# Optimization experiments

Measured on AMD Instinct MI355X. Metric: run time of the kernel, lower is better.

Reference implementation:

```python
import jax, jax.numpy as jnp
import numpy as np

POOLED_SIZES = [12, 16, 20, 24]
NUM_HEADS = 8
EPS_LN = 1e-5


def _pool_mat(in_size, out_size):
    # torch adaptive_avg_pool1d/2d semantics as an averaging matrix [out, in]
    m = np.zeros((out_size, in_size), np.float32)
    for i in range(out_size):
        s = (i * in_size) // out_size
        e = -((-(i + 1) * in_size) // out_size)  # ceil
        m[i, s:e] = 1.0 / (e - s)
    return jnp.asarray(m)


def _dwconv(x, w, b):
    # depthwise 3x3, stride 1, padding 1 (NCHW, OIHW with I=1)
    y = jax.lax.conv_general_dilated(
        x, w, (1, 1), 'SAME', feature_group_count=x.shape[1],
        dimension_numbers=('NCHW', 'OIHW', 'NCHW'))
    return y + b[None, :, None, None]


def _ln(x, g, b):
    m = x.mean(-1, keepdims=True)
    v = jnp.mean((x - m) ** 2, axis=-1, keepdims=True)
    return (x - m) / jnp.sqrt(v + EPS_LN) * g + b


def setup_inputs() -> dict:
    key = jax.random.key(0)
    ks = jax.random.split(key, 16)
    B, H, W, C = 4, 56, 56, 256
    hid = 4 * C
    nrm = lambda k, shape, s=0.02: jax.random.normal(k, shape, jnp.float32) * s
    inp = {
        'x': jax.random.normal(ks[0], (B, H * W, C), jnp.float32),
        'cpe_w': nrm(ks[1], (C, 1, 3, 3)), 'cpe_b': jnp.zeros((C,), jnp.float32),
        'norm1_w': jnp.ones((C,), jnp.float32), 'norm1_b': jnp.zeros((C,), jnp.float32),
        'q_w': nrm(ks[2], (C, C)),
        'kv_w': nrm(ks[3], (2 * C, C)),
        'attn_norm_w': jnp.ones((C,), jnp.float32), 'attn_norm_b': jnp.zeros((C,), jnp.float32),
        'proj_w': nrm(ks[4], (C, C)), 'proj_b': jnp.zeros((C,), jnp.float32),
        'norm2_w': jnp.ones((C,), jnp.float32), 'norm2_b': jnp.zeros((C,), jnp.float32),
        'fc1_w': nrm(ks[5], (hid, C)), 'fc1_b': jnp.zeros((hid,), jnp.float32),
        'irb_conv_w': nrm(ks[6], (hid, 1, 3, 3)), 'irb_conv_b': jnp.zeros((hid,), jnp.float32),
        'fc2_w': nrm(ks[7], (C, hid)), 'fc2_b': jnp.zeros((C,), jnp.float32),
        'H': H, 'W': W,
    }
    for i in range(4):
        inp[f'dconv{i}_w'] = nrm(ks[8 + i], (C, 1, 3, 3))
        inp[f'dconv{i}_b'] = jnp.zeros((C,), jnp.float32)
    return inp


def _forward(x, cpe_w, cpe_b, norm1_w, norm1_b, q_w, kv_w, attn_norm_w, attn_norm_b,
             proj_w, proj_b, dconv0_w, dconv0_b, dconv1_w, dconv1_b, dconv2_w, dconv2_b,
             dconv3_w, dconv3_b, norm2_w, norm2_b, fc1_w, fc1_b, irb_conv_w, irb_conv_b,
             fc2_w, fc2_b, H, W):
    B, N, C = x.shape
    nh = NUM_HEADS
    hd = C // nh
    scale = hd ** -0.5
    # conditional positional encoding: x = cpe(x) + x
    xi = x.transpose(0, 2, 1).reshape(B, C, H, W)
    xi = _dwconv(xi, cpe_w, cpe_b) + xi
    x = xi.reshape(B, C, N).transpose(0, 2, 1)
    # ---- pyramid pooling attention ----
    xn = _ln(x, norm1_w, norm1_b)
    q = (xn @ q_w.T).reshape(B, N, nh, hd).transpose(0, 2, 1, 3)  # [B,nh,N,hd]
    x_ = xn.transpose(0, 2, 1).reshape(B, C, H, W)
    dws = [(dconv0_w, dconv0_b), (dconv1_w, dconv1_b),
           (dconv2_w, dconv2_b), (dconv3_w, dconv3_b)]
    pools = []
    for p, (dw, db) in zip(POOLED_SIZES, dws):
        ph = _pool_mat(H, p)
        pw = _pool_mat(W, p)
        pool = jnp.einsum('oi,bcij,pj->bcop', ph, x_, pw)  # adaptive avg pool (p,p)
        pool = pool + _dwconv(pool, dw, db)
        pools.append(pool.reshape(B, C, -1))
    pools = jnp.concatenate(pools, axis=2).transpose(0, 2, 1)  # [B,P,C], P=1376
    pools = _ln(pools, attn_norm_w, attn_norm_b)
    kv = (pools @ kv_w.T).reshape(B, -1, 2, nh, hd).transpose(2, 0, 3, 1, 4)
    k, v = kv[0], kv[1]  # [B,nh,P,hd]
    attn = jax.nn.softmax(jnp.einsum('bhnd,bhpd->bhnp', q, k) * scale, axis=-1)
    out = jnp.einsum('bhnp,bhpd->bhnd', attn, v).transpose(0, 2, 1, 3).reshape(B, N, C)
    out = out @ proj_w.T + proj_b
    x = x + out
    # ---- IRB FFN ----
    xn = _ln(x, norm2_w, norm2_b)
    xi = xn.transpose(0, 2, 1).reshape(B, C, H, W)
    h = jnp.einsum('oc,bchw->bohw', fc1_w, xi) + fc1_b[None, :, None, None]
    h = jax.nn.gelu(h, approximate=False)
    h = h + _dwconv(h, irb_conv_w, irb_conv_b)
    o = jnp.einsum('oc,bchw->bohw', fc2_w, h) + fc2_b[None, :, None, None]
    x = x + o.reshape(B, C, N).transpose(0, 2, 1)
    return x


def reference(x, cpe_w, cpe_b, norm1_w, norm1_b, q_w, kv_w, attn_norm_w, attn_norm_b,
              proj_w, proj_b, dconv0_w, dconv0_b, dconv1_w, dconv1_b, dconv2_w, dconv2_b,
              dconv3_w, dconv3_b, norm2_w, norm2_b, fc1_w, fc1_b, irb_conv_w, irb_conv_b,
              fc2_w, fc2_b, H, W):
    return _forward(x, cpe_w, cpe_b, norm1_w, norm1_b, q_w, kv_w, attn_norm_w, attn_norm_b,
                    proj_w, proj_b, dconv0_w, dconv0_b, dconv1_w, dconv1_b, dconv2_w, dconv2_b,
                    dconv3_w, dconv3_b, norm2_w, norm2_b, fc1_w, fc1_b, irb_conv_w, irb_conv_b,
                    fc2_w, fc2_b, H, W)
```

## Files before the change

kernel.cpp:

```cpp
#include <hip/hip_runtime.h>
#include <hip/hip_bf16.h>

#define BQ 4
#define HH 56
#define WW 56
#define NN (HH*WW)
#define CC 256
#define NHEAD 8
#define HD 32
#define PP 1376
#define PPAD 1408
#define HIDN 1024
#define EPS_LN 1e-5f
#define QSCALE_LOG2E 0.25503484f

typedef unsigned short bf16u;
typedef __attribute__((ext_vector_type(8))) short short8;
typedef __attribute__((ext_vector_type(4))) float f32x4;

__device__ __forceinline__ float bf2f(bf16u u){
  union { unsigned int i; float f; } v; v.i = ((unsigned int)u) << 16; return v.f;
}
__device__ __forceinline__ bf16u f2bf(float f){
  unsigned int x = __float_as_uint(f);
  x += 0x7fffu + ((x >> 16) & 1u);
  return (bf16u)(x >> 16);
}
__device__ __forceinline__ bf16u f2bf_r(float f){
  return (bf16u)((__float_as_uint(f) + 0x8000u) >> 16);
}
__device__ __forceinline__ void cvt4(const ushort4 u, float* d){
  d[0]=bf2f(u.x); d[1]=bf2f(u.y); d[2]=bf2f(u.z); d[3]=bf2f(u.w);
}

#define CSEG 4
__global__ void k_init(const float* __restrict__ qw, const float* __restrict__ kvw,
                       const float* __restrict__ pw, const float* __restrict__ f1,
                       const float* __restrict__ f2, bf16u* __restrict__ wo,
                       const float* __restrict__ x, const float* __restrict__ w,
                       const float* __restrict__ bias, const float* __restrict__ g,
                       const float* __restrict__ be, float* __restrict__ x1,
                       bf16u* __restrict__ xnb){
  if (blockIdx.x < 768){
    int off = (blockIdx.x*256 + threadIdx.x) * 4;
    const float* s;
    if (off < 65536)       s = qw  + off;
    else if (off < 196608) s = kvw + off - 65536;
    else if (off < 262144) s = pw  + off - 196608;
    else if (off < 524288) s = f1  + off - 262144;
    else                   s = f2  + off - 524288;
    float4 v = *(const float4*)s;
    ushort4 u = {f2bf(v.x), f2bf(v.y), f2bf(v.z), f2bf(v.w)};
    *(ushort4*)(wo + off) = u;
    return;
  }
  int t = threadIdx.x;
  int wave = t >> 6, lane = t & 63;
  int widx = (blockIdx.x - 768)*4 + wave;
  const int nseg = WW/CSEG;
  int xseg = widx % nseg;
  int y    = (widx / nseg) % HH;
  int b    = widx / (nseg*HH);
  int c0 = lane*4;
  int x0 = xseg*CSEG;
  float wv[36];
  {
    const float* wp = w + (size_t)c0*9;
#pragma unroll
    for (int i = 0; i < 9; i++){
      float4 v = *(const float4*)(wp + i*4);
      wv[i*4+0]=v.x; wv[i*4+1]=v.y; wv[i*4+2]=v.z; wv[i*4+3]=v.w;
    }
  }
  float4 bi4 = *(const float4*)&bias[c0];
  float bi[4] = {bi4.x, bi4.y, bi4.z, bi4.w};
  float4 gv = *(const float4*)&g[c0];
  float4 bv = *(const float4*)&be[c0];
  const float* rowc = x + ((size_t)b*NN + (size_t)y*WW)*CC + c0;
  const float* rowm = (y > 0)    ? rowc - (size_t)WW*CC : rowc;
  const float* rowp = (y < HH-1) ? rowc + (size_t)WW*CC : rowc;
  if (y == 0){
#pragma unroll
    for (int cc = 0; cc < 4; cc++){ wv[cc*9+0]=0.f; wv[cc*9+1]=0.f; wv[cc*9+2]=0.f; }
  }
  if (y == HH-1){
#pragma unroll
    for (int cc = 0; cc < 4; cc++){ wv[cc*9+6]=0.f; wv[cc*9+7]=0.f; wv[cc*9+8]=0.f; }
  }
  float win[3][3][4];
  float4 rawA[3], rawB[3];
  if (x0 == 0){
#pragma unroll
    for (int r = 0; r < 3; r++)
#pragma unroll
      for (int cc = 0; cc < 4; cc++) win[0][r][cc] = 0.f;
  } else {
    size_t o = (size_t)(x0-1)*CC;
    float4 a0 = *(const float4*)&rowm[o];
    float4 a1 = *(const float4*)&rowc[o];
    float4 a2 = *(const float4*)&rowp[o];
    win[0][0][0]=a0.x; win[0][0][1]=a0.y; win[0][0][2]=a0.z; win[0][0][3]=a0.w;
    win[0][1][0]=a1.x; win[0][1][1]=a1.y; win[0][1][2]=a1.z; win[0][1][3]=a1.w;
    win[0][2][0]=a2.x; win[0][2][1]=a2.y; win[0][2][2]=a2.z; win[0][2][3]=a2.w;
  }
  {
    size_t o = (size_t)x0*CC;
    float4 a0 = *(const float4*)&rowm[o];
    float4 a1 = *(const float4*)&rowc[o];
    float4 a2 = *(const float4*)&rowp[o];
    win[1][0][0]=a0.x; win[1][0][1]=a0.y; win[1][0][2]=a0.z; win[1][0][3]=a0.w;
    win[1][1][0]=a1.x; win[1][1][1]=a1.y; win[1][1][2]=a1.z; win[1][1][3]=a1.w;
    win[1][2][0]=a2.x; win[1][2][1]=a2.y; win[1][2][2]=a2.z; win[1][2][3]=a2.w;
  }
  {
    size_t o = (size_t)(x0+1)*CC;
    rawA[0] = *(const float4*)&rowm[o];
    rawA[1] = *(const float4*)&rowc[o];
    rawA[2] = *(const float4*)&rowp[o];
  }
#pragma unroll
  for (int xx = 0; xx < CSEG; xx++){
    float4* cur = (xx & 1) ? rawB : rawA;
    float4* nxt = (xx & 1) ? rawA : rawB;
    if (xx < CSEG-1){
      int xg = x0 + xx + 2;
      if (xg < WW){
        size_t o = (size_t)xg*CC;
        nxt[0] = *(const float4*)&rowm[o];
        nxt[1] = *(const float4*)&rowc[o];
        nxt[2] = *(const float4*)&rowp[o];
      } else {
        float4 z = {0.f,0.f,0.f,0.f};
        nxt[0] = z; nxt[1] = z; nxt[2] = z;
      }
    }
    int sl2 = (xx+2)%3, slm = xx%3, slc = (xx+1)%3;
#pragma unroll
    for (int r = 0; r < 3; r++){
      win[sl2][r][0]=cur[r].x; win[sl2][r][1]=cur[r].y;
      win[sl2][r][2]=cur[r].z; win[sl2][r][3]=cur[r].w;
    }
    float o4[4];
#pragma unroll
    for (int cc = 0; cc < 4; cc++){
      float a = bi[cc];
      a += win[slm][0][cc]*wv[cc*9+0] + win[slc][0][cc]*wv[cc*9+1] + win[sl2][0][cc]*wv[cc*9+2];
      a += win[slm][1][cc]*wv[cc*9+3] + win[slc][1][cc]*wv[cc*9+4] + win[sl2][1][cc]*wv[cc*9+5];
      a += win[slm][2][cc]*wv[cc*9+6] + win[slc][2][cc]*wv[cc*9+7] + win[sl2][2][cc]*wv[cc*9+8];
      o4[cc] = win[slc][1][cc] + a;
    }
    size_t pix = (size_t)b*NN + (size_t)y*WW + x0 + xx;
    float4 ov = {o4[0],o4[1],o4[2],o4[3]};
    *(float4*)&x1[pix*CC + c0] = ov;
    float s  = o4[0]+o4[1]+o4[2]+o4[3];
    float s2 = o4[0]*o4[0]+o4[1]*o4[1]+o4[2]*o4[2]+o4[3]*o4[3];
#pragma unroll
    for (int off = 32; off; off >>= 1){
      s  += __shfl_xor(s,  off);
      s2 += __shfl_xor(s2, off);
    }
    float mean = s * (1.f/CC);
    float var  = s2 * (1.f/CC) - mean*mean;
    float rstd = rsqrtf(var + EPS_LN);
    float y0 = (o4[0]-mean)*rstd*gv.x + bv.x;
    float y1 = (o4[1]-mean)*rstd*gv.y + bv.y;
    float y2 = (o4[2]-mean)*rstd*gv.z + bv.z;
    float y3 = (o4[3]-mean)*rstd*gv.w + bv.w;
    ushort4 yb = {f2bf_r(y0), f2bf_r(y1), f2bf_r(y2), f2bf_r(y3)};
    *(ushort4*)&xnb[pix*CC + c0] = yb;
  }
}

__global__ void k_ln_bf16(const float* __restrict__ X, const float* __restrict__ g,
                          const float* __restrict__ be, bf16u* __restrict__ Y){
  int wave = threadIdx.x >> 6, lane = threadIdx.x & 63;
  int row = blockIdx.x*4 + wave;
  int c0 = lane*4;
  float4 v = *(const float4*)&X[(size_t)row*CC + c0];
  float s  = v.x+v.y+v.z+v.w;
  float s2 = v.x*v.x+v.y*v.y+v.z*v.z+v.w*v.w;
#pragma unroll
  for (int off = 32; off; off >>= 1){
    s  += __shfl_xor(s,  off);
    s2 += __shfl_xor(s2, off);
  }
  float mean = s * (1.f/CC);
  float var  = s2 * (1.f/CC) - mean*mean;
  float rstd = rsqrtf(var + EPS_LN);
  float4 gv = *(const float4*)&g[c0];
  float4 bv = *(const float4*)&be[c0];
  ushort4 yb = {f2bf_r((v.x-mean)*rstd*gv.x + bv.x),
                f2bf_r((v.y-mean)*rstd*gv.y + bv.y),
                f2bf_r((v.z-mean)*rstd*gv.z + bv.z),
                f2bf_r((v.w-mean)*rstd*gv.w + bv.w)};
  *(ushort4*)&Y[(size_t)row*CC + c0] = yb;
}

__global__ void k_pool(const bf16u* __restrict__ xnb, float* __restrict__ praw){
  int bp = blockIdx.x;
  int b = bp / PP, p = bp % PP;
  int ps, pi;
  if (p < 144)      { ps = 12; pi = p; }
  else if (p < 400) { ps = 16; pi = p - 144; }
  else if (p < 800) { ps = 20; pi = p - 400; }
  else              { ps = 24; pi = p - 800; }
  int oi = pi / ps, oj = pi % ps;
  int si = oi*HH/ps, ei = ((oi+1)*HH + ps - 1)/ps;
  int sj = oj*WW/ps, ej = ((oj+1)*WW + ps - 1)/ps;
  int c = threadIdx.x;
  const bf16u* xb = xnb + (size_t)b*NN*CC + c;
  float acc = 0.f;
  for (int i = si; i < ei; i++)
    for (int j = sj; j < ej; j++)
      acc += bf2f(xb[(size_t)(i*WW+j)*CC]);
  praw[(size_t)bp*CC + c] = acc / (float)((ei-si)*(ej-sj));
}

__global__ void k_pooldw_ln(const float* __restrict__ praw,
    const float* w0, const float* b0, const float* w1, const float* b1,
    const float* w2, const float* b2, const float* w3, const float* b3,
    const float* __restrict__ g, const float* __restrict__ be,
    bf16u* __restrict__ pools){
  int bp = blockIdx.x;
  int b = bp / PP, p = bp % PP;
  int ps, pi, off; const float *w, *bi;
  if (p < 144)      { ps=12; pi=p;     off=0;   w=w0; bi=b0; }
  else if (p < 400) { ps=16; pi=p-144; off=144; w=w1; bi=b1; }
  else if (p < 800) { ps=20; pi=p-400; off=400; w=w2; bi=b2; }
  else              { ps=24; pi=p-800; off=800; w=w3; bi=b3; }
  int oi = pi/ps, oj = pi%ps;
  int c = threadIdx.x;
  const float* base = praw + (size_t)(b*PP + off)*CC + c;
  float acc = bi[c];
#pragma unroll
  for (int kh = 0; kh < 3; kh++){
    int ii = oi + kh - 1; if (ii < 0 || ii >= ps) continue;
#pragma unroll
    for (int kw = 0; kw < 3; kw++){
      int jj = oj + kw - 1; if (jj < 0 || jj >= ps) continue;
      acc += base[(size_t)(ii*ps+jj)*CC] * w[c*9 + kh*3 + kw];
    }
  }
  float v = base[(size_t)(oi*ps+oj)*CC] + acc;
  float s = v, s2 = v*v;
#pragma unroll
  for (int o2_ = 32; o2_; o2_ >>= 1){
    s  += __shfl_down(s,  o2_);
    s2 += __shfl_down(s2, o2_);
  }
  __shared__ float red[10];
  int wv_ = c >> 6, ln = c & 63;
  if (ln == 0){ red[wv_] = s; red[4+wv_] = s2; }
  __syncthreads();
  if (c == 0){
    float S  = red[0]+red[1]+red[2]+red[3];
    float S2 = red[4]+red[5]+red[6]+red[7];
    float mean = S * (1.f/CC);
    float var  = S2 * (1.f/CC) - mean*mean;
    red[8] = mean; red[9] = rsqrtf(var + EPS_LN);
  }
  __syncthreads();
  float mean = red[8], rstd = red[9];
  pools[(size_t)bp*CC + c] = f2bf_r((v - mean) * rstd * g[c] + be[c]);
}

#define GST 40
template<int MT, int NT, bool OUT_BF16, bool HAS_BIAS, bool DO_GELU, bool HAS_RES, bool VT_OUT>
__global__ __launch_bounds__(256) void k_gemm_mfma(const bf16u* __restrict__ A,
                       const bf16u* __restrict__ Wt,
                       const float* __restrict__ bias, void* Outp,
                       const float* Res, bf16u* __restrict__ vtout,
                       int M, int Nout, int K, float oscale){
  constexpr int MW = (MT == 128) ? 4 : 2;
  constexpr int NW = (NT == 128) ? 4 : 2;
  __shared__ bf16u Ash[2][MT*GST];
  __shared__ bf16u Bsh[2][NT*GST];
  int t = threadIdx.x;
  int wave = t >> 6, lane = t & 63, quad = lane >> 4, l16 = lane & 15;
  int m0 = blockIdx.y * MT, n0 = blockIdx.x * NT;
  int wm = (wave >> 1) * (MT/2);
  int wn = (wave & 1) * (NT/2);
  int ar = (MT==128) ? (t>>1) : (t>>2);
  int ac = (MT==128) ? ((t&1)*16) : ((t&3)*8);
  int br = (NT==128) ? (t>>1) : (t>>2);
  int bc = (NT==128) ? ((t&1)*16) : ((t&3)*8);
  int astore = ar*GST + ac;
  int bstore = br*GST + bc;
  const bf16u* ap = A  + (size_t)(m0+ar)*K + ac;
  const bf16u* bp = Wt + (size_t)(n0+br)*K + bc;

  {
    uint4 t0 = *(const uint4*)ap;
    *(uint4*)&Ash[0][astore] = t0;
    if constexpr (MT == 128){ uint4 t1 = *(const uint4*)(ap+8); *(uint4*)&Ash[0][astore+8] = t1; }
    uint4 t2 = *(const uint4*)bp;
    *(uint4*)&Bsh[0][bstore] = t2;
    if constexpr (NT == 128){ uint4 t3 = *(const uint4*)(bp+8); *(uint4*)&Bsh[0][bstore+8] = t3; }
  }
  uint4 aA0, aA1, bA0, bA1;
  uint4 aB0, aB1, bB0, bB1;
  ap += 32; bp += 32;
  aA0 = *(const uint4*)ap;
  if constexpr (MT == 128) aA1 = *(const uint4*)(ap+8);
  bA0 = *(const uint4*)bp;
  if constexpr (NT == 128) bA1 = *(const uint4*)(bp+8);
  ap += 32; bp += 32;
  aB0 = *(const uint4*)ap;
  if constexpr (MT == 128) aB1 = *(const uint4*)(ap+8);
  bB0 = *(const uint4*)bp;
  if constexpr (NT == 128) bB1 = *(const uint4*)(bp+8);
  ap += 32; bp += 32;
  __syncthreads();

  f32x4 zero = {0.f,0.f,0.f,0.f};
  f32x4 acc[MW][NW];
#pragma unroll
  for (int i = 0; i < MW; i++)
#pragma unroll
    for (int j = 0; j < NW; j++) acc[i][j] = zero;

  int nks = K >> 5;

#define GEMM_STEP(BUF) { \
    short8 af[MW], bfr[NW]; \
    _Pragma("unroll") \
    for (int mi = 0; mi < MW; mi++) \
      af[mi] = *(const short8*)&Ash[BUF][(wm + mi*16 + l16)*GST + quad*8]; \
    _Pragma("unroll") \
    for (int ni = 0; ni < NW; ni++) \
      bfr[ni] = *(const short8*)&Bsh[BUF][(wn + ni*16 + l16)*GST + quad*8]; \
    _Pragma("unroll") \
    for (int mi = 0; mi < MW; mi++) \
      _Pragma("unroll") \
      for (int ni = 0; ni < NW; ni++) \
        acc[mi][ni] = __builtin_amdgcn_mfma_f32_16x16x32_bf16(af[mi], bfr[ni], acc[mi][ni], 0,0,0); }

  for (int ks = 0; ks < nks; ks += 2){
    if (ks < nks-1){
      *(uint4*)&Ash[1][astore] = aA0;
      if constexpr (MT == 128) *(uint4*)&Ash[1][astore+8] = aA1;
      *(uint4*)&Bsh[1][bstore] = bA0;
      if constexpr (NT == 128) *(uint4*)&Bsh[1][bstore+8] = bA1;
      if (ks < nks-3){
        aA0 = *(const uint4*)ap;
        if constexpr (MT == 128) aA1 = *(const uint4*)(ap+8);
        bA0 = *(const uint4*)bp;
        if constexpr (NT == 128) bA1 = *(const uint4*)(bp+8);
        ap += 32; bp += 32;
      }
    }
    GEMM_STEP(0)
    if (ks < nks-1) __syncthreads();
    if (ks+1 < nks-1){
      *(uint4*)&Ash[0][astore] = aB0;
      if constexpr (MT == 128) *(uint4*)&Ash[0][astore+8] = aB1;
      *(uint4*)&Bsh[0][bstore] = bB0;
      if constexpr (NT == 128) *(uint4*)&Bsh[0][bstore+8] = bB1;
      if (ks+1 < nks-3){
        aB0 = *(const uint4*)ap;
        if constexpr (MT == 128) aB1 = *(const uint4*)(ap+8);
        bB0 = *(const uint4*)bp;
        if constexpr (NT == 128) bB1 = *(const uint4*)(bp+8);
        ap += 32; bp += 32;
      }
    }
    if (ks+1 < nks){
      GEMM_STEP(1)
      if (ks+1 < nks-1) __syncthreads();
    }
  }
#undef GEMM_STEP

#pragma unroll
  for (int mi = 0; mi < MW; mi++){
#pragma unroll
    for (int r = 0; r < 4; r++){
      int row = m0 + wm + mi*16 + quad*4 + r;
#pragma unroll
      for (int ni = 0; ni < NW; ni++){
        int col = n0 + wn + ni*16 + l16;
        float v = acc[mi][ni][r] * oscale;
        if constexpr (HAS_BIAS) v += bias[col];
        if constexpr (DO_GELU)  v = 0.5f*v*(1.f + erff(v*0.70710678118654752f));
        if constexpr (HAS_RES)  v += Res[(size_t)row*Nout + col];
        if constexpr (VT_OUT){
          if (col < CC){
            ((bf16u*)Outp)[(size_t)row*Nout + col] = f2bf_r(v);
          } else {
            int bb = row / PP, pp = row - bb*PP;
            vtout[((size_t)(bb*CC + (col - CC)))*PPAD + pp] = f2bf_r(v);
          }
        } else if constexpr (OUT_BF16){
          ((bf16u*)Outp)[(size_t)row*Nout + col] = f2bf_r(v);
        } else {
          ((float*)Outp)[(size_t)row*Nout + col] = v;
        }
      }
    }
  }
}

#define KST 40
#define VST 72
__global__ __launch_bounds__(256) void k_attn_mfma(const bf16u* __restrict__ q,
                       const bf16u* __restrict__ kvb, const bf16u* __restrict__ vt,
                       bf16u* __restrict__ out){
  __shared__ bf16u Ksh[2][64*KST];
  __shared__ bf16u Vsh[2][32*VST];
  int t = threadIdx.x;
  int wave = t >> 6, lane = t & 63, quad = lane >> 4, l16 = lane & 15;
  int bid = blockIdx.x;
  int qt = bid % (NN/64);
  int h  = (bid / (NN/64)) % NHEAD;
  int b  = bid / ((NN/64)*NHEAD);
  int q0 = qt*64 + wave*16;
  const bf16u* qptr = q + (size_t)(b*NN + q0 + l16)*CC + h*HD + quad*8;
  short8 qf = *(const short8*)qptr;
  f32x4 zero = {0.f,0.f,0.f,0.f};
  f32x4 o0 = zero, o1 = zero, osum = zero;
  const short8 onesf = {0x3F80,0x3F80,0x3F80,0x3F80,0x3F80,0x3F80,0x3F80,0x3F80};
  int ksr = t >> 2, ksc = (t & 3) * 8;
  int vsr = t >> 3, vsc = (t & 7) * 8;
  const bf16u* ksrc = kvb + (size_t)(b*PP + ksr)*(2*CC) + h*HD + ksc;
  const bf16u* vsrc = vt  + (size_t)(b*CC + h*HD + vsr)*PPAD + vsc;
  int krow = (ksr & 32) | ((ksr & 4) << 2) | ((ksr & 24) >> 1) | (ksr & 3);
  int kstore = krow*KST + ksc;
  int vstore = vsr*VST + vsc;
  int koffA = l16*KST + quad*8;
  int koffB = koffA + 16*KST;
  int voff0 = l16*VST + quad*8;
  int voff1 = (16 + l16)*VST + quad*8;

  uint4 kreg = *(const uint4*)ksrc;
  uint4 vreg = *(const uint4*)vsrc;
  *(uint4*)&Ksh[0][kstore] = kreg;
  *(uint4*)&Vsh[0][vstore] = vreg;
  ksrc += (size_t)64*(2*CC); vsrc += 64;
  kreg = *(const uint4*)ksrc; vreg = *(const uint4*)vsrc;
  __syncthreads();

#define PAIR(KB, VB, cb) { \
    short8 kfa = *(const short8*)&KB[cb*KST + koffA]; \
    short8 kfb = *(const short8*)&KB[cb*KST + koffB]; \
    f32x4 sa = __builtin_amdgcn_mfma_f32_16x16x32_bf16(kfa, qf, zero, 0,0,0); \
    f32x4 sb = __builtin_amdgcn_mfma_f32_16x16x32_bf16(kfb, qf, zero, 0,0,0); \
    float ea0 = __builtin_amdgcn_exp2f(sa[0]), ea1 = __builtin_amdgcn_exp2f(sa[1]); \
    float ea2 = __builtin_amdgcn_exp2f(sa[2]), ea3 = __builtin_amdgcn_exp2f(sa[3]); \
    float eb0 = __builtin_amdgcn_exp2f(sb[0]), eb1 = __builtin_amdgcn_exp2f(sb[1]); \
    float eb2 = __builtin_amdgcn_exp2f(sb[2]), eb3 = __builtin_amdgcn_exp2f(sb[3]); \
    unsigned ra0 = __float_as_uint(ea0) + 0x8000u, ra1 = __float_as_uint(ea1) + 0x8000u; \
    unsigned ra2 = __float_as_uint(ea2) + 0x8000u, ra3 = __float_as_uint(ea3) + 0x8000u; \
    unsigned rb0 = __float_as_uint(eb0) + 0x8000u, rb1 = __float_as_uint(eb1) + 0x8000u; \
    unsigned rb2 = __float_as_uint(eb2) + 0x8000u, rb3 = __float_as_uint(eb3) + 0x8000u; \
    union { uint4 u; short8 s; } pk; \
    pk.u.x = __builtin_amdgcn_perm(ra1, ra0, 0x07060302u); \
    pk.u.y = __builtin_amdgcn_perm(ra3, ra2, 0x07060302u); \
    pk.u.z = __builtin_amdgcn_perm(rb1, rb0, 0x07060302u); \
    pk.u.w = __builtin_amdgcn_perm(rb3, rb2, 0x07060302u); \
    short8 pa = pk.s; \
    short8 vf0 = *(const short8*)&VB[cb + voff0]; \
    short8 vf1 = *(const short8*)&VB[cb + voff1]; \
    o0 = __builtin_amdgcn_mfma_f32_16x16x32_bf16(pa, vf0, o0, 0,0,0); \
    o1 = __builtin_amdgcn_mfma_f32_16x16x32_bf16(pa, vf1, o1, 0,0,0); \
    osum = __builtin_amdgcn_mfma_f32_16x16x32_bf16(pa, onesf, osum, 0,0,0); }

  for (int ch = 0; ch < PPAD/64 - 1; ch++){
    int cur = ch & 1;
    bf16u* KB = &Ksh[cur][0];
    bf16u* VB = &Vsh[cur][0];
    *(uint4*)&Ksh[cur^1][kstore] = kreg;
    *(uint4*)&Vsh[cur^1][vstore] = vreg;
    if (ch < PPAD/64 - 2){
      ksrc += (size_t)64*(2*CC); vsrc += 64;
      kreg = *(const uint4*)ksrc; vreg = *(const uint4*)vsrc;
    }
    PAIR(KB, VB, 0)
    PAIR(KB, VB, 32)
    __syncthreads();
  }
  {
    bf16u* KB = &Ksh[1][0];
    bf16u* VB = &Vsh[1][0];
    PAIR(KB, VB, 0)
  }
#undef PAIR

#pragma unroll
  for (int r = 0; r < 4; r++){
    int qq = quad*4 + r;
    float inv = 1.f / osum[r];
    size_t base = (size_t)(b*NN + q0 + qq)*CC + h*HD;
    out[base + l16]      = f2bf_r(o0[r]*inv);
    out[base + 16 + l16] = f2bf_r(o1[r]*inv);
  }
}

#define DWSEG 8
__global__ __launch_bounds__(256) void k_dwh(const bf16u* __restrict__ h, const float* __restrict__ w,
                      const float* __restrict__ bias, bf16u* __restrict__ h2){
  const int nseg = WW/DWSEG;
  int bid = blockIdx.x;
  int xseg = bid % nseg;
  int y    = (bid / nseg) % HH;
  int b    = bid / (nseg*HH);
  int t = threadIdx.x;
  int c0 = t*4;
  int x0 = xseg*DWSEG;
  float wv[36];
  {
    const float4* wp = (const float4*)(w + (size_t)c0*9);
#pragma unroll
    for (int i = 0; i < 9; i++){
      float4 v = wp[i];
      wv[i*4+0]=v.x; wv[i*4+1]=v.y; wv[i*4+2]=v.z; wv[i*4+3]=v.w;
    }
  }
  float4 bi4 = *(const float4*)&bias[c0];
  float bi[4] = {bi4.x, bi4.y, bi4.z, bi4.w};
  const bf16u* rowc = h + ((size_t)b*NN + (size_t)y*WW)*HIDN + c0;
  const bf16u* rowm = (y > 0)    ? rowc - (size_t)WW*HIDN : rowc;
  const bf16u* rowp = (y < HH-1) ? rowc + (size_t)WW*HIDN : rowc;
  if (y == 0){
#pragma unroll
    for (int cc = 0; cc < 4; cc++){ wv[cc*9+0]=0.f; wv[cc*9+1]=0.f; wv[cc*9+2]=0.f; }
  }
  if (y == HH-1){
#pragma unroll
    for (int cc = 0; cc < 4; cc++){ wv[cc*9+6]=0.f; wv[cc*9+7]=0.f; wv[cc*9+8]=0.f; }
  }
  float win[3][3][4];
  ushort4 rawA[3], rawB[3];
  if (x0 == 0){
#pragma unroll
    for (int r = 0; r < 3; r++)
#pragma unroll
      for (int cc = 0; cc < 4; cc++) win[0][r][cc] = 0.f;
  } else {
    size_t o = (size_t)(x0-1)*HIDN;
    ushort4 a0 = *(const ushort4*)&rowm[o];
    ushort4 a1 = *(const ushort4*)&rowc[o];
    ushort4 a2 = *(const ushort4*)&rowp[o];
    cvt4(a0, win[0][0]); cvt4(a1, win[0][1]); cvt4(a2, win[0][2]);
  }
  {
    size_t o = (size_t)x0*HIDN;
    ushort4 a0 = *(const ushort4*)&rowm[o];
    ushort4 a1 = *(const ushort4*)&rowc[o];
    ushort4 a2 = *(const ushort4*)&rowp[o];
    cvt4(a0, win[1][0]); cvt4(a1, win[1][1]); cvt4(a2, win[1][2]);
  }
  {
    size_t o = (size_t)(x0+1)*HIDN;
    rawA[0] = *(const ushort4*)&rowm[o];
    rawA[1] = *(const ushort4*)&rowc[o];
    rawA[2] = *(const ushort4*)&rowp[o];
  }
#pragma unroll
  for (int x = 0; x < DWSEG; x++){
    ushort4* cur = (x & 1) ? rawB : rawA;
    ushort4* nxt = (x & 1) ? rawA : rawB;
    if (x < DWSEG-1){
      int xg = x0 + x + 2;
      if (xg < WW){
        size_t o = (size_t)xg*HIDN;
        nxt[0] = *(const ushort4*)&rowm[o];
        nxt[1] = *(const ushort4*)&rowc[o];
        nxt[2] = *(const ushort4*)&rowp[o];
      } else {
        ushort4 z = {0,0,0,0};
        nxt[0] = z; nxt[1] = z; nxt[2] = z;
      }
    }
    int s2 = (x+2)%3, sm = x%3, sc_ = (x+1)%3;
    cvt4(cur[0], win[s2][0]); cvt4(cur[1], win[s2][1]); cvt4(cur[2], win[s2][2]);
    float o0[4];
#pragma unroll
    for (int cc = 0; cc < 4; cc++){
      float a = bi[cc];
      a += win[sm][0][cc]*wv[cc*9+0] + win[sc_][0][cc]*wv[cc*9+1] + win[s2][0][cc]*wv[cc*9+2];
      a += win[sm][1][cc]*wv[cc*9+3] + win[sc_][1][cc]*wv[cc*9+4] + win[s2][1][cc]*wv[cc*9+5];
      a += win[sm][2][cc]*wv[cc*9+6] + win[sc_][2][cc]*wv[cc*9+7] + win[s2][2][cc]*wv[cc*9+8];
      o0[cc] = win[sc_][1][cc] + a;
    }
    ushort4 ou = {f2bf_r(o0[0]), f2bf_r(o0[1]), f2bf_r(o0[2]), f2bf_r(o0[3])};
    *(ushort4*)&h2[((size_t)b*NN + (size_t)y*WW + x0 + x)*HIDN + c0] = ou;
  }
}

extern "C" void kernel_launch(void* const* d_in, const int* in_sizes, int n_in,
                              void* d_out, int out_size, void* d_ws, size_t ws_size,
                              hipStream_t stream){
  const float* x      = (const float*)d_in[0];
  const float* cpe_w  = (const float*)d_in[1];
  const float* cpe_b  = (const float*)d_in[2];
  const float* n1w    = (const float*)d_in[3];
  const float* n1b    = (const float*)d_in[4];
  const float* q_w    = (const float*)d_in[5];
  const float* kv_w   = (const float*)d_in[6];
  const float* anw    = (const float*)d_in[7];
  const float* anb    = (const float*)d_in[8];
  const float* proj_w = (const float*)d_in[9];
  const float* proj_b = (const float*)d_in[10];
  const float* n2w    = (const float*)d_in[11];
  const float* n2b    = (const float*)d_in[12];
  const float* fc1_w  = (const float*)d_in[13];
  const float* fc1_b  = (const float*)d_in[14];
  const float* irb_w  = (const float*)d_in[15];
  const float* irb_b  = (const float*)d_in[16];
  const float* fc2_w  = (const float*)d_in[17];
  const float* fc2_b  = (const float*)d_in[18];
  const float* dw0    = (const float*)d_in[21];
  const float* db0    = (const float*)d_in[22];
  const float* dw1    = (const float*)d_in[23];
  const float* db1    = (const float*)d_in[24];
  const float* dw2    = (const float*)d_in[25];
  const float* db2    = (const float*)d_in[26];
  const float* dw3    = (const float*)d_in[27];
  const float* db3    = (const float*)d_in[28];

  const size_t BNC = (size_t)BQ*NN*CC;
  const size_t BPC = (size_t)BQ*PP*CC;
  const size_t BNH = (size_t)BQ*NN*HIDN;

  float* x1   = (float*)d_ws;
  bf16u* xnb  = (bf16u*)(x1 + BNC);
  bf16u* wbuf = xnb + BNC;
  bf16u* wq   = wbuf;
  bf16u* wkv  = wbuf + 65536;
  bf16u* wpj  = wbuf + 196608;
  bf16u* wf1  = wbuf + 262144;
  bf16u* wf2  = wbuf + 524288;
  float* A0   = (float*)(wbuf + 786432);
  bf16u* qb   = (bf16u*)A0;
  float* praw = (float*)(qb + BNC);
  bf16u* poolsb = (bf16u*)(praw + BPC);
  bf16u* kvb  = poolsb + BPC;
  bf16u* vtb  = kvb + (size_t)BQ*PP*2*CC;
  bf16u* hbuf = (bf16u*)A0;
  bf16u* h2buf = hbuf + BNH;

  k_init<<<768 + (BQ*HH*(WW/CSEG))/4, 256, 0, stream>>>(q_w, kv_w, proj_w, fc1_w, fc2_w, wbuf,
                                            x, cpe_w, cpe_b, n1w, n1b, x1, xnb);
  k_gemm_mfma<64,64,true,false,false,false,false><<<dim3(CC/64, BQ*NN/64), 256, 0, stream>>>(
      xnb, wq, nullptr, qb, nullptr, nullptr, BQ*NN, CC, CC, QSCALE_LOG2E);
  k_pool<<<BQ*PP, 256, 0, stream>>>(xnb, praw);
  k_pooldw_ln<<<BQ*PP, 256, 0, stream>>>(praw, dw0,db0, dw1,db1, dw2,db2, dw3,db3,
                                         anw, anb, poolsb);
  k_gemm_mfma<64,64,true,false,false,false,true><<<dim3(2*CC/64, BQ*PP/64), 256, 0, stream>>>(
      poolsb, wkv, nullptr, kvb, nullptr, vtb, BQ*PP, 2*CC, CC, 1.0f);
  k_attn_mfma<<<BQ*NHEAD*(NN/64), 256, 0, stream>>>(qb, kvb, vtb, qb);
  k_gemm_mfma<64,64,false,true,false,true,false><<<dim3(CC/64, BQ*NN/64), 256, 0, stream>>>(
      qb, wpj, proj_b, x1, x1, nullptr, BQ*NN, CC, CC, 1.0f);
  k_ln_bf16<<<BQ*NN/4, 256, 0, stream>>>(x1, n2w, n2b, xnb);
  k_gemm_mfma<128,128,true,true,true,false,false><<<dim3(HIDN/128, BQ*NN/128), 256, 0, stream>>>(
      xnb, wf1, fc1_b, hbuf, nullptr, nullptr, BQ*NN, HIDN, CC, 1.0f);
  k_dwh<<<BQ*HH*(WW/DWSEG), 256, 0, stream>>>(hbuf, irb_w, irb_b, h2buf);
  k_gemm_mfma<64,64,false,true,false,true,false><<<dim3(CC/64, BQ*NN/64), 256, 0, stream>>>(
      h2buf, wf2, fc2_b, d_out, x1, nullptr, BQ*NN, CC, HIDN, 1.0f);
}
```

Measured before the change: 308.5 us.

## Process 32 queries per wave in attention and vectorize pooling per wave

The attention kernel now runs 2 waves per block, each handling 32 queries (two 16-row MFMA tiles). Each K/V fragment loaded from LDS is reused twice, and the per-block K/V tile load is shared across half as many waves. The pooling kernel now assigns one pooled cell per wave with 4-wide vector loads instead of one cell per block with scalar loads. In exchange, the attention kernel uses more registers per wave and has fewer waves per block to hide latency.

```diff
diff --git a/kernel.cpp b/kernel.cpp
--- a/kernel.cpp
+++ b/kernel.cpp
@@ -197,7 +197,8 @@
 }
 
 __global__ void k_pool(const bf16u* __restrict__ xnb, float* __restrict__ praw){
-  int bp = blockIdx.x;
+  int wave = threadIdx.x >> 6, lane = threadIdx.x & 63;
+  int bp = blockIdx.x*4 + wave;
   int b = bp / PP, p = bp % PP;
   int ps, pi;
   if (p < 144)      { ps = 12; pi = p; }
@@ -207,13 +208,17 @@
   int oi = pi / ps, oj = pi % ps;
   int si = oi*HH/ps, ei = ((oi+1)*HH + ps - 1)/ps;
   int sj = oj*WW/ps, ej = ((oj+1)*WW + ps - 1)/ps;
-  int c = threadIdx.x;
-  const bf16u* xb = xnb + (size_t)b*NN*CC + c;
-  float acc = 0.f;
+  int c0 = lane*4;
+  const bf16u* xb = xnb + (size_t)b*NN*CC + c0;
+  float a0=0.f, a1=0.f, a2=0.f, a3=0.f;
   for (int i = si; i < ei; i++)
-    for (int j = sj; j < ej; j++)
-      acc += bf2f(xb[(size_t)(i*WW+j)*CC]);
-  praw[(size_t)bp*CC + c] = acc / (float)((ei-si)*(ej-sj));
+    for (int j = sj; j < ej; j++){
+      ushort4 v = *(const ushort4*)&xb[(size_t)(i*WW+j)*CC];
+      a0 += bf2f(v.x); a1 += bf2f(v.y); a2 += bf2f(v.z); a3 += bf2f(v.w);
+    }
+  float inv = 1.f / (float)((ei-si)*(ej-sj));
+  float4 o = {a0*inv, a1*inv, a2*inv, a3*inv};
+  *(float4*)&praw[(size_t)bp*CC + c0] = o;
 }
 
 __global__ void k_pooldw_ln(const float* __restrict__ praw,
@@ -402,7 +407,7 @@
 
 #define KST 40
 #define VST 72
-__global__ __launch_bounds__(256) void k_attn_mfma(const bf16u* __restrict__ q,
+__global__ __launch_bounds__(128) void k_attn_mfma(const bf16u* __restrict__ q,
                        const bf16u* __restrict__ kvb, const bf16u* __restrict__ vt,
                        bf16u* __restrict__ out){
   __shared__ bf16u Ksh[2][64*KST];
@@ -413,14 +418,16 @@
   int qt = bid % (NN/64);
   int h  = (bid / (NN/64)) % NHEAD;
   int b  = bid / ((NN/64)*NHEAD);
-  int q0 = qt*64 + wave*16;
+  int q0 = qt*64 + wave*32;
   const bf16u* qptr = q + (size_t)(b*NN + q0 + l16)*CC + h*HD + quad*8;
-  short8 qf = *(const short8*)qptr;
+  short8 qf0 = *(const short8*)qptr;
+  short8 qf1 = *(const short8*)(qptr + (size_t)16*CC);
   f32x4 zero = {0.f,0.f,0.f,0.f};
-  f32x4 o0 = zero, o1 = zero, osum = zero;
+  f32x4 o00 = zero, o01 = zero, o10 = zero, o11 = zero;
+  f32x4 osum0 = zero, osum1 = zero;
   const short8 onesf = {0x3F80,0x3F80,0x3F80,0x3F80,0x3F80,0x3F80,0x3F80,0x3F80};
-  int ksr = t >> 2, ksc = (t & 3) * 8;
-  int vsr = t >> 3, vsc = (t & 7) * 8;
+  int ksr = t >> 1, ksc = (t & 1) * 16;
+  int vsr = t >> 2, vsc = (t & 3) * 16;
   const bf16u* ksrc = kvb + (size_t)(b*PP + ksr)*(2*CC) + h*HD + ksc;
   const bf16u* vsrc = vt  + (size_t)(b*CC + h*HD + vsr)*PPAD + vsc;
   int krow = (ksr & 32) | ((ksr & 4) << 2) | ((ksr & 24) >> 1) | (ksr & 3);
@@ -431,48 +438,71 @@
   int voff0 = l16*VST + quad*8;
   int voff1 = (16 + l16)*VST + quad*8;
 
-  uint4 kreg = *(const uint4*)ksrc;
-  uint4 vreg = *(const uint4*)vsrc;
-  *(uint4*)&Ksh[0][kstore] = kreg;
-  *(uint4*)&Vsh[0][vstore] = vreg;
+  uint4 ka = *(const uint4*)ksrc, kb2 = *(const uint4*)(ksrc+8);
+  uint4 va = *(const uint4*)vsrc, vb2 = *(const uint4*)(vsrc+8);
+  *(uint4*)&Ksh[0][kstore]     = ka;
+  *(uint4*)&Ksh[0][kstore + 8] = kb2;
+  *(uint4*)&Vsh[0][vstore]     = va;
+  *(uint4*)&Vsh[0][vstore + 8] = vb2;
   ksrc += (size_t)64*(2*CC); vsrc += 64;
-  kreg = *(const uint4*)ksrc; vreg = *(const uint4*)vsrc;
+  ka = *(const uint4*)ksrc; kb2 = *(const uint4*)(ksrc+8);
+  va = *(const uint4*)vsrc; vb2 = *(const uint4*)(vsrc+8);
   __syncthreads();
 
 #define PAIR(KB, VB, cb) { \
     short8 kfa = *(const short8*)&KB[cb*KST + koffA]; \
     short8 kfb = *(const short8*)&KB[cb*KST + koffB]; \
-    f32x4 sa = __builtin_amdgcn_mfma_f32_16x16x32_bf16(kfa, qf, zero, 0,0,0); \
-    f32x4 sb = __builtin_amdgcn_mfma_f32_16x16x32_bf16(kfb, qf, zero, 0,0,0); \
-    float ea0 = __builtin_amdgcn_exp2f(sa[0]), ea1 = __builtin_amdgcn_exp2f(sa[1]); \
-    float ea2 = __builtin_amdgcn_exp2f(sa[2]), ea3 = __builtin_amdgcn_exp2f(sa[3]); \
-    float eb0 = __builtin_amdgcn_exp2f(sb[0]), eb1 = __builtin_amdgcn_exp2f(sb[1]); \
-    float eb2 = __builtin_amdgcn_exp2f(sb[2]), eb3 = __builtin_amdgcn_exp2f(sb[3]); \
-    unsigned ra0 = __float_as_uint(ea0) + 0x8000u, ra1 = __float_as_uint(ea1) + 0x8000u; \
-    unsigned ra2 = __float_as_uint(ea2) + 0x8000u, ra3 = __float_as_uint(ea3) + 0x8000u; \
-    unsigned rb0 = __float_as_uint(eb0) + 0x8000u, rb1 = __float_as_uint(eb1) + 0x8000u; \
-    unsigned rb2 = __float_as_uint(eb2) + 0x8000u, rb3 = __float_as_uint(eb3) + 0x8000u; \
-    union { uint4 u; short8 s; } pk; \
-    pk.u.x = __builtin_amdgcn_perm(ra1, ra0, 0x07060302u); \
-    pk.u.y = __builtin_amdgcn_perm(ra3, ra2, 0x07060302u); \
-    pk.u.z = __builtin_amdgcn_perm(rb1, rb0, 0x07060302u); \
-    pk.u.w = __builtin_amdgcn_perm(rb3, rb2, 0x07060302u); \
-    short8 pa = pk.s; \
+    f32x4 sa0 = __builtin_amdgcn_mfma_f32_16x16x32_bf16(kfa, qf0, zero, 0,0,0); \
+    f32x4 sb0 = __builtin_amdgcn_mfma_f32_16x16x32_bf16(kfb, qf0, zero, 0,0,0); \
+    f32x4 sa1 = __builtin_amdgcn_mfma_f32_16x16x32_bf16(kfa, qf1, zero, 0,0,0); \
+    f32x4 sb1 = __builtin_amdgcn_mfma_f32_16x16x32_bf16(kfb, qf1, zero, 0,0,0); \
+    float e00 = __builtin_amdgcn_exp2f(sa0[0]), e01 = __builtin_amdgcn_exp2f(sa0[1]); \
+    float e02 = __builtin_amdgcn_exp2f(sa0[2]), e03 = __builtin_amdgcn_exp2f(sa0[3]); \
+    float e04 = __builtin_amdgcn_exp2f(sb0[0]), e05 = __builtin_amdgcn_exp2f(sb0[1]); \
+    float e06 = __builtin_amdgcn_exp2f(sb0[2]), e07 = __builtin_amdgcn_exp2f(sb0[3]); \
+    float e10 = __builtin_amdgcn_exp2f(sa1[0]), e11 = __builtin_amdgcn_exp2f(sa1[1]); \
+    float e12 = __builtin_amdgcn_exp2f(sa1[2]), e13 = __builtin_amdgcn_exp2f(sa1[3]); \
+    float e14 = __builtin_amdgcn_exp2f(sb1[0]), e15 = __builtin_amdgcn_exp2f(sb1[1]); \
+    float e16 = __builtin_amdgcn_exp2f(sb1[2]), e17 = __builtin_amdgcn_exp2f(sb1[3]); \
+    unsigned r00 = __float_as_uint(e00)+0x8000u, r01 = __float_as_uint(e01)+0x8000u; \
+    unsigned r02 = __float_as_uint(e02)+0x8000u, r03 = __float_as_uint(e03)+0x8000u; \
+    unsigned r04 = __float_as_uint(e04)+0x8000u, r05 = __float_as_uint(e05)+0x8000u; \
+    unsigned r06 = __float_as_uint(e06)+0x8000u, r07 = __float_as_uint(e07)+0x8000u; \
+    unsigned r10 = __float_as_uint(e10)+0x8000u, r11 = __float_as_uint(e11)+0x8000u; \
+    unsigned r12 = __float_as_uint(e12)+0x8000u, r13 = __float_as_uint(e13)+0x8000u; \
+    unsigned r14 = __float_as_uint(e14)+0x8000u, r15 = __float_as_uint(e15)+0x8000u; \
+    unsigned r16 = __float_as_uint(e16)+0x8000u, r17 = __float_as_uint(e17)+0x8000u; \
+    union { uint4 u; short8 s; } pk0, pk1; \
+    pk0.u.x = __builtin_amdgcn_perm(r01, r00, 0x07060302u); \
+    pk0.u.y = __builtin_amdgcn_perm(r03, r02, 0x07060302u); \
+    pk0.u.z = __builtin_amdgcn_perm(r05, r04, 0x07060302u); \
+    pk0.u.w = __builtin_amdgcn_perm(r07, r06, 0x07060302u); \
+    pk1.u.x = __builtin_amdgcn_perm(r11, r10, 0x07060302u); \
+    pk1.u.y = __builtin_amdgcn_perm(r13, r12, 0x07060302u); \
+    pk1.u.z = __builtin_amdgcn_perm(r15, r14, 0x07060302u); \
+    pk1.u.w = __builtin_amdgcn_perm(r17, r16, 0x07060302u); \
+    short8 pa0 = pk0.s, pa1 = pk1.s; \
     short8 vf0 = *(const short8*)&VB[cb + voff0]; \
     short8 vf1 = *(const short8*)&VB[cb + voff1]; \
-    o0 = __builtin_amdgcn_mfma_f32_16x16x32_bf16(pa, vf0, o0, 0,0,0); \
-    o1 = __builtin_amdgcn_mfma_f32_16x16x32_bf16(pa, vf1, o1, 0,0,0); \
-    osum = __builtin_amdgcn_mfma_f32_16x16x32_bf16(pa, onesf, osum, 0,0,0); }
+    o00 = __builtin_amdgcn_mfma_f32_16x16x32_bf16(pa0, vf0, o00, 0,0,0); \
+    o01 = __builtin_amdgcn_mfma_f32_16x16x32_bf16(pa0, vf1, o01, 0,0,0); \
+    o10 = __builtin_amdgcn_mfma_f32_16x16x32_bf16(pa1, vf0, o10, 0,0,0); \
+    o11 = __builtin_amdgcn_mfma_f32_16x16x32_bf16(pa1, vf1, o11, 0,0,0); \
+    osum0 = __builtin_amdgcn_mfma_f32_16x16x32_bf16(pa0, onesf, osum0, 0,0,0); \
+    osum1 = __builtin_amdgcn_mfma_f32_16x16x32_bf16(pa1, onesf, osum1, 0,0,0); }
 
   for (int ch = 0; ch < PPAD/64 - 1; ch++){
     int cur = ch & 1;
     bf16u* KB = &Ksh[cur][0];
     bf16u* VB = &Vsh[cur][0];
-    *(uint4*)&Ksh[cur^1][kstore] = kreg;
-    *(uint4*)&Vsh[cur^1][vstore] = vreg;
+    *(uint4*)&Ksh[cur^1][kstore]     = ka;
+    *(uint4*)&Ksh[cur^1][kstore + 8] = kb2;
+    *(uint4*)&Vsh[cur^1][vstore]     = va;
+    *(uint4*)&Vsh[cur^1][vstore + 8] = vb2;
     if (ch < PPAD/64 - 2){
       ksrc += (size_t)64*(2*CC); vsrc += 64;
-      kreg = *(const uint4*)ksrc; vreg = *(const uint4*)vsrc;
+      ka = *(const uint4*)ksrc; kb2 = *(const uint4*)(ksrc+8);
+      va = *(const uint4*)vsrc; vb2 = *(const uint4*)(vsrc+8);
     }
     PAIR(KB, VB, 0)
     PAIR(KB, VB, 32)
@@ -488,10 +518,14 @@
 #pragma unroll
   for (int r = 0; r < 4; r++){
     int qq = quad*4 + r;
-    float inv = 1.f / osum[r];
-    size_t base = (size_t)(b*NN + q0 + qq)*CC + h*HD;
-    out[base + l16]      = f2bf_r(o0[r]*inv);
-    out[base + 16 + l16] = f2bf_r(o1[r]*inv);
+    float inv0 = 1.f / osum0[r];
+    float inv1 = 1.f / osum1[r];
+    size_t base0 = (size_t)(b*NN + q0 + qq)*CC + h*HD;
+    size_t base1 = base0 + (size_t)16*CC;
+    out[base0 + l16]      = f2bf_r(o00[r]*inv0);
+    out[base0 + 16 + l16] = f2bf_r(o01[r]*inv0);
+    out[base1 + l16]      = f2bf_r(o10[r]*inv1);
+    out[base1 + 16 + l16] = f2bf_r(o11[r]*inv1);
   }
 }
 
@@ -643,12 +677,12 @@
                                             x, cpe_w, cpe_b, n1w, n1b, x1, xnb);
   k_gemm_mfma<64,64,true,false,false,false,false><<<dim3(CC/64, BQ*NN/64), 256, 0, stream>>>(
       xnb, wq, nullptr, qb, nullptr, nullptr, BQ*NN, CC, CC, QSCALE_LOG2E);
-  k_pool<<<BQ*PP, 256, 0, stream>>>(xnb, praw);
+  k_pool<<<BQ*PP/4, 256, 0, stream>>>(xnb, praw);
   k_pooldw_ln<<<BQ*PP, 256, 0, stream>>>(praw, dw0,db0, dw1,db1, dw2,db2, dw3,db3,
                                          anw, anb, poolsb);
   k_gemm_mfma<64,64,true,false,false,false,true><<<dim3(2*CC/64, BQ*PP/64), 256, 0, stream>>>(
       poolsb, wkv, nullptr, kvb, nullptr, vtb, BQ*PP, 2*CC, CC, 1.0f);
-  k_attn_mfma<<<BQ*NHEAD*(NN/64), 256, 0, stream>>>(qb, kvb, vtb, qb);
+  k_attn_mfma<<<BQ*NHEAD*(NN/64), 128, 0, stream>>>(qb, kvb, vtb, qb);
   k_gemm_mfma<64,64,false,true,false,true,false><<<dim3(CC/64, BQ*NN/64), 256, 0, stream>>>(
       qb, wpj, proj_b, x1, x1, nullptr, BQ*NN, CC, CC, 1.0f);
   k_ln_bf16<<<BQ*NN/4, 256, 0, stream>>>(x1, n2w, n2b, xnb);
```

Result: no change. 310.8 us (+0.7%).

## Merge Q projection GEMM and adaptive pooling into one heterogeneous launch

Applied to the files above, without the earlier changes.

Refactors the GEMM into a device-side body that takes explicit block indices and shared buffers. A new combined kernel runs the Q-projection GEMM blocks and the pooling blocks side by side in one grid. Pooling is also reworked so each wave handles one pooled cell, with 4 channels per lane loaded as vectors. This removes a launch boundary and lets the GEMM and pooling work overlap, at the cost of a mixed-role grid whose block imbalance can hurt scheduling.

```diff
diff --git a/kernel.cpp b/kernel.cpp
--- a/kernel.cpp
+++ b/kernel.cpp
@@ -196,88 +196,21 @@
   *(ushort4*)&Y[(size_t)row*CC + c0] = yb;
 }
 
-__global__ void k_pool(const bf16u* __restrict__ xnb, float* __restrict__ praw){
-  int bp = blockIdx.x;
-  int b = bp / PP, p = bp % PP;
-  int ps, pi;
-  if (p < 144)      { ps = 12; pi = p; }
-  else if (p < 400) { ps = 16; pi = p - 144; }
-  else if (p < 800) { ps = 20; pi = p - 400; }
-  else              { ps = 24; pi = p - 800; }
-  int oi = pi / ps, oj = pi % ps;
-  int si = oi*HH/ps, ei = ((oi+1)*HH + ps - 1)/ps;
-  int sj = oj*WW/ps, ej = ((oj+1)*WW + ps - 1)/ps;
-  int c = threadIdx.x;
-  const bf16u* xb = xnb + (size_t)b*NN*CC + c;
-  float acc = 0.f;
-  for (int i = si; i < ei; i++)
-    for (int j = sj; j < ej; j++)
-      acc += bf2f(xb[(size_t)(i*WW+j)*CC]);
-  praw[(size_t)bp*CC + c] = acc / (float)((ei-si)*(ej-sj));
-}
-
-__global__ void k_pooldw_ln(const float* __restrict__ praw,
-    const float* w0, const float* b0, const float* w1, const float* b1,
-    const float* w2, const float* b2, const float* w3, const float* b3,
-    const float* __restrict__ g, const float* __restrict__ be,
-    bf16u* __restrict__ pools){
-  int bp = blockIdx.x;
-  int b = bp / PP, p = bp % PP;
-  int ps, pi, off; const float *w, *bi;
-  if (p < 144)      { ps=12; pi=p;     off=0;   w=w0; bi=b0; }
-  else if (p < 400) { ps=16; pi=p-144; off=144; w=w1; bi=b1; }
-  else if (p < 800) { ps=20; pi=p-400; off=400; w=w2; bi=b2; }
-  else              { ps=24; pi=p-800; off=800; w=w3; bi=b3; }
-  int oi = pi/ps, oj = pi%ps;
-  int c = threadIdx.x;
-  const float* base = praw + (size_t)(b*PP + off)*CC + c;
-  float acc = bi[c];
-#pragma unroll
-  for (int kh = 0; kh < 3; kh++){
-    int ii = oi + kh - 1; if (ii < 0 || ii >= ps) continue;
-#pragma unroll
-    for (int kw = 0; kw < 3; kw++){
-      int jj = oj + kw - 1; if (jj < 0 || jj >= ps) continue;
-      acc += base[(size_t)(ii*ps+jj)*CC] * w[c*9 + kh*3 + kw];
-    }
-  }
-  float v = base[(size_t)(oi*ps+oj)*CC] + acc;
-  float s = v, s2 = v*v;
-#pragma unroll
-  for (int o2_ = 32; o2_; o2_ >>= 1){
-    s  += __shfl_down(s,  o2_);
-    s2 += __shfl_down(s2, o2_);
-  }
-  __shared__ float red[10];
-  int wv_ = c >> 6, ln = c & 63;
-  if (ln == 0){ red[wv_] = s; red[4+wv_] = s2; }
-  __syncthreads();
-  if (c == 0){
-    float S  = red[0]+red[1]+red[2]+red[3];
-    float S2 = red[4]+red[5]+red[6]+red[7];
-    float mean = S * (1.f/CC);
-    float var  = S2 * (1.f/CC) - mean*mean;
-    red[8] = mean; red[9] = rsqrtf(var + EPS_LN);
-  }
-  __syncthreads();
-  float mean = red[8], rstd = red[9];
-  pools[(size_t)bp*CC + c] = f2bf_r((v - mean) * rstd * g[c] + be[c]);
-}
-
 #define GST 40
 template<int MT, int NT, bool OUT_BF16, bool HAS_BIAS, bool DO_GELU, bool HAS_RES, bool VT_OUT>
-__global__ __launch_bounds__(256) void k_gemm_mfma(const bf16u* __restrict__ A,
-                       const bf16u* __restrict__ Wt,
+__device__ __forceinline__ void gemm_body(int bx, int by,
+                       const bf16u* __restrict__ A, const bf16u* __restrict__ Wt,
                        const float* __restrict__ bias, void* Outp,
                        const float* Res, bf16u* __restrict__ vtout,
-                       int M, int Nout, int K, float oscale){
+                       int Nout, int K, float oscale,
+                       bf16u* __restrict__ AshB, bf16u* __restrict__ BshB){
   constexpr int MW = (MT == 128) ? 4 : 2;
   constexpr int NW = (NT == 128) ? 4 : 2;
-  __shared__ bf16u Ash[2][MT*GST];
-  __shared__ bf16u Bsh[2][NT*GST];
+  bf16u* Ash0 = AshB; bf16u* Ash1 = AshB + MT*GST;
+  bf16u* Bsh0 = BshB; bf16u* Bsh1 = BshB + NT*GST;
   int t = threadIdx.x;
   int wave = t >> 6, lane = t & 63, quad = lane >> 4, l16 = lane & 15;
-  int m0 = blockIdx.y * MT, n0 = blockIdx.x * NT;
+  int m0 = by * MT, n0 = bx * NT;
   int wm = (wave >> 1) * (MT/2);
   int wn = (wave & 1) * (NT/2);
   int ar = (MT==128) ? (t>>1) : (t>>2);
@@ -291,11 +224,11 @@
 
   {
     uint4 t0 = *(const uint4*)ap;
-    *(uint4*)&Ash[0][astore] = t0;
-    if constexpr (MT == 128){ uint4 t1 = *(const uint4*)(ap+8); *(uint4*)&Ash[0][astore+8] = t1; }
+    *(uint4*)&Ash0[astore] = t0;
+    if constexpr (MT == 128){ uint4 t1 = *(const uint4*)(ap+8); *(uint4*)&Ash0[astore+8] = t1; }
     uint4 t2 = *(const uint4*)bp;
-    *(uint4*)&Bsh[0][bstore] = t2;
-    if constexpr (NT == 128){ uint4 t3 = *(const uint4*)(bp+8); *(uint4*)&Bsh[0][bstore+8] = t3; }
+    *(uint4*)&Bsh0[bstore] = t2;
+    if constexpr (NT == 128){ uint4 t3 = *(const uint4*)(bp+8); *(uint4*)&Bsh0[bstore+8] = t3; }
   }
   uint4 aA0, aA1, bA0, bA1;
   uint4 aB0, aB1, bB0, bB1;
@@ -321,14 +254,14 @@
 
   int nks = K >> 5;
 
-#define GEMM_STEP(BUF) { \
+#define GEMM_STEP(AshP, BshP) { \
     short8 af[MW], bfr[NW]; \
     _Pragma("unroll") \
     for (int mi = 0; mi < MW; mi++) \
-      af[mi] = *(const short8*)&Ash[BUF][(wm + mi*16 + l16)*GST + quad*8]; \
+      af[mi] = *(const short8*)&AshP[(wm + mi*16 + l16)*GST + quad*8]; \
     _Pragma("unroll") \
     for (int ni = 0; ni < NW; ni++) \
-      bfr[ni] = *(const short8*)&Bsh[BUF][(wn + ni*16 + l16)*GST + quad*8]; \
+      bfr[ni] = *(const short8*)&BshP[(wn + ni*16 + l16)*GST + quad*8]; \
     _Pragma("unroll") \
     for (int mi = 0; mi < MW; mi++) \
       _Pragma("unroll") \
@@ -337,10 +270,10 @@
 
   for (int ks = 0; ks < nks; ks += 2){
     if (ks < nks-1){
-      *(uint4*)&Ash[1][astore] = aA0;
-      if constexpr (MT == 128) *(uint4*)&Ash[1][astore+8] = aA1;
-      *(uint4*)&Bsh[1][bstore] = bA0;
-      if constexpr (NT == 128) *(uint4*)&Bsh[1][bstore+8] = bA1;
+      *(uint4*)&Ash1[astore] = aA0;
+      if constexpr (MT == 128) *(uint4*)&Ash1[astore+8] = aA1;
+      *(uint4*)&Bsh1[bstore] = bA0;
+      if constexpr (NT == 128) *(uint4*)&Bsh1[bstore+8] = bA1;
       if (ks < nks-3){
         aA0 = *(const uint4*)ap;
         if constexpr (MT == 128) aA1 = *(const uint4*)(ap+8);
@@ -349,13 +282,13 @@
         ap += 32; bp += 32;
       }
     }
-    GEMM_STEP(0)
+    GEMM_STEP(Ash0, Bsh0)
     if (ks < nks-1) __syncthreads();
     if (ks+1 < nks-1){
-      *(uint4*)&Ash[0][astore] = aB0;
-      if constexpr (MT == 128) *(uint4*)&Ash[0][astore+8] = aB1;
-      *(uint4*)&Bsh[0][bstore] = bB0;
-      if constexpr (NT == 128) *(uint4*)&Bsh[0][bstore+8] = bB1;
+      *(uint4*)&Ash0[astore] = aB0;
+      if constexpr (MT == 128) *(uint4*)&Ash0[astore+8] = aB1;
+      *(uint4*)&Bsh0[bstore] = bB0;
+      if constexpr (NT == 128) *(uint4*)&Bsh0[bstore+8] = bB1;
       if (ks+1 < nks-3){
         aB0 = *(const uint4*)ap;
         if constexpr (MT == 128) aB1 = *(const uint4*)(ap+8);
@@ -365,7 +298,7 @@
       }
     }
     if (ks+1 < nks){
-      GEMM_STEP(1)
+      GEMM_STEP(Ash1, Bsh1)
       if (ks+1 < nks-1) __syncthreads();
     }
   }
@@ -398,6 +331,105 @@
       }
     }
   }
+}
+
+template<int MT, int NT, bool OUT_BF16, bool HAS_BIAS, bool DO_GELU, bool HAS_RES, bool VT_OUT>
+__global__ __launch_bounds__(256) void k_gemm_mfma(const bf16u* __restrict__ A,
+                       const bf16u* __restrict__ Wt,
+                       const float* __restrict__ bias, void* Outp,
+                       const float* Res, bf16u* __restrict__ vtout,
+                       int M, int Nout, int K, float oscale){
+  __shared__ bf16u Ash[2][MT*GST];
+  __shared__ bf16u Bsh[2][NT*GST];
+  gemm_body<MT,NT,OUT_BF16,HAS_BIAS,DO_GELU,HAS_RES,VT_OUT>(
+      blockIdx.x, blockIdx.y, A, Wt, bias, Outp, Res, vtout, Nout, K, oscale,
+      &Ash[0][0], &Bsh[0][0]);
+}
+
+#define QGRID ((CC/64)*(BQ*NN/64))
+__global__ __launch_bounds__(256) void k_qpool(const bf16u* __restrict__ xnb,
+                       const bf16u* __restrict__ wq, bf16u* __restrict__ qb,
+                       float* __restrict__ praw){
+  __shared__ bf16u Ash[2][64*GST];
+  __shared__ bf16u Bsh[2][64*GST];
+  if (blockIdx.x < QGRID){
+    int bx = blockIdx.x % (CC/64);
+    int by = blockIdx.x / (CC/64);
+    gemm_body<64,64,true,false,false,false,false>(
+        bx, by, xnb, wq, nullptr, qb, nullptr, nullptr, CC, CC, QSCALE_LOG2E,
+        &Ash[0][0], &Bsh[0][0]);
+    return;
+  }
+  int wave = threadIdx.x >> 6, lane = threadIdx.x & 63;
+  int bp = (blockIdx.x - QGRID)*4 + wave;
+  int b = bp / PP, p = bp % PP;
+  int ps, pi;
+  if (p < 144)      { ps = 12; pi = p; }
+  else if (p < 400) { ps = 16; pi = p - 144; }
+  else if (p < 800) { ps = 20; pi = p - 400; }
+  else              { ps = 24; pi = p - 800; }
+  int oi = pi / ps, oj = pi % ps;
+  int si = oi*HH/ps, ei = ((oi+1)*HH + ps - 1)/ps;
+  int sj = oj*WW/ps, ej = ((oj+1)*WW + ps - 1)/ps;
+  int c0 = lane*4;
+  const bf16u* xb = xnb + (size_t)b*NN*CC + c0;
+  float a0=0.f, a1=0.f, a2=0.f, a3=0.f;
+  for (int i = si; i < ei; i++)
+    for (int j = sj; j < ej; j++){
+      ushort4 v = *(const ushort4*)&xb[(size_t)(i*WW+j)*CC];
+      a0 += bf2f(v.x); a1 += bf2f(v.y); a2 += bf2f(v.z); a3 += bf2f(v.w);
+    }
+  float inv = 1.f / (float)((ei-si)*(ej-sj));
+  float4 o = {a0*inv, a1*inv, a2*inv, a3*inv};
+  *(float4*)&praw[(size_t)bp*CC + c0] = o;
+}
+
+__global__ void k_pooldw_ln(const float* __restrict__ praw,
+    const float* w0, const float* b0, const float* w1, const float* b1,
+    const float* w2, const float* b2, const float* w3, const float* b3,
+    const float* __restrict__ g, const float* __restrict__ be,
+    bf16u* __restrict__ pools){
+  int bp = blockIdx.x;
+  int b = bp / PP, p = bp % PP;
+  int ps, pi, off; const float *w, *bi;
+  if (p < 144)      { ps=12; pi=p;     off=0;   w=w0; bi=b0; }
+  else if (p < 400) { ps=16; pi=p-144; off=144; w=w1; bi=b1; }
+  else if (p < 800) { ps=20; pi=p-400; off=400; w=w2; bi=b2; }
+  else              { ps=24; pi=p-800; off=800; w=w3; bi=b3; }
+  int oi = pi/ps, oj = pi%ps;
+  int c = threadIdx.x;
+  const float* base = praw + (size_t)(b*PP + off)*CC + c;
+  float acc = bi[c];
+#pragma unroll
+  for (int kh = 0; kh < 3; kh++){
+    int ii = oi + kh - 1; if (ii < 0 || ii >= ps) continue;
+#pragma unroll
+    for (int kw = 0; kw < 3; kw++){
+      int jj = oj + kw - 1; if (jj < 0 || jj >= ps) continue;
+      acc += base[(size_t)(ii*ps+jj)*CC] * w[c*9 + kh*3 + kw];
+    }
+  }
+  float v = base[(size_t)(oi*ps+oj)*CC] + acc;
+  float s = v, s2 = v*v;
+#pragma unroll
+  for (int o2_ = 32; o2_; o2_ >>= 1){
+    s  += __shfl_down(s,  o2_);
+    s2 += __shfl_down(s2, o2_);
+  }
+  __shared__ float red[10];
+  int wv_ = c >> 6, ln = c & 63;
+  if (ln == 0){ red[wv_] = s; red[4+wv_] = s2; }
+  __syncthreads();
+  if (c == 0){
+    float S  = red[0]+red[1]+red[2]+red[3];
+    float S2 = red[4]+red[5]+red[6]+red[7];
+    float mean = S * (1.f/CC);
+    float var  = S2 * (1.f/CC) - mean*mean;
+    red[8] = mean; red[9] = rsqrtf(var + EPS_LN);
+  }
+  __syncthreads();
+  float mean = red[8], rstd = red[9];
+  pools[(size_t)bp*CC + c] = f2bf_r((v - mean) * rstd * g[c] + be[c]);
 }
 
 #define KST 40
@@ -641,9 +673,7 @@
 
   k_init<<<768 + (BQ*HH*(WW/CSEG))/4, 256, 0, stream>>>(q_w, kv_w, proj_w, fc1_w, fc2_w, wbuf,
                                             x, cpe_w, cpe_b, n1w, n1b, x1, xnb);
-  k_gemm_mfma<64,64,true,false,false,false,false><<<dim3(CC/64, BQ*NN/64), 256, 0, stream>>>(
-      xnb, wq, nullptr, qb, nullptr, nullptr, BQ*NN, CC, CC, QSCALE_LOG2E);
-  k_pool<<<BQ*PP, 256, 0, stream>>>(xnb, praw);
+  k_qpool<<<QGRID + BQ*PP/4, 256, 0, stream>>>(xnb, wq, qb, praw);
   k_pooldw_ln<<<BQ*PP, 256, 0, stream>>>(praw, dw0,db0, dw1,db1, dw2,db2, dw3,db3,
                                          anw, anb, poolsb);
   k_gemm_mfma<64,64,true,false,false,false,true><<<dim3(2*CC/64, BQ*PP/64), 256, 0, stream>>>(
```

Measured after the change: 300.5 us. 1.03x faster.
